# Kernel tuning notes

Hardware: AMD Instinct MI355X
Metric: run time of the kernel (lower is better)

Reference implementation:

```python
import jax, jax.numpy as jnp
import numpy as np

B, S, E, L = 4, 4096, 64, 3
INIT_SCALE = 0.03


def setup_inputs() -> dict:
    key = jax.random.key(0)
    ks = jax.random.split(key, 7)
    return {
        "x": jax.random.normal(ks[0], (B, S, S + 1), dtype=jnp.float32),
        "q_ws": jax.random.normal(ks[1], (L, E, E), dtype=jnp.float32) * INIT_SCALE,
        "k_ws": jax.random.normal(ks[2], (L, E, E), dtype=jnp.float32) * INIT_SCALE,
        "v_ws": jax.random.normal(ks[3], (L, E, E), dtype=jnp.float32) * INIT_SCALE,
        "random_matrix": jax.random.normal(ks[4], (S, E - 1), dtype=jnp.float32) * INIT_SCALE,
        "coeffs_attended": jax.random.normal(ks[5], (S, E), dtype=jnp.float32) * INIT_SCALE,
        "offset": jax.random.normal(ks[6], (1,), dtype=jnp.float32),
    }


def reference(x, q_ws, k_ws, v_ws, random_matrix, coeffs_attended, offset):
    seq_length = random_matrix.shape[0]
    # project first seq_length feature columns, keep the last column raw -> [B, S, E]
    av = jnp.concatenate(
        [jnp.einsum('bsf,fe->bse', x[:, :, :seq_length], random_matrix), x[:, :, -1:]],
        axis=2,
    )

    def layer(av, ws):
        qw, kw, vw = ws
        q = jnp.einsum('bse,ed->bsd', av, qw)   # [B, S, E]
        k = jnp.einsum('bse,ed->bsd', av, kw)
        v = jnp.einsum('bse,ed->bsd', av, vw)
        scores = jax.nn.softmax(jnp.einsum('bqd,bkd->bqk', q, k), axis=-1)  # [B, S, S]
        out = jnp.einsum('bqk,bkd->bqd', scores, v)
        # skip_connections=False: output replaces attended values
        return out, None

    av, _ = jax.lax.scan(layer, av, (q_ws, k_ws, v_ws))
    final = jnp.einsum('bij,ij->b', av, coeffs_attended)  # [B]
    return final + offset[0]
```

## Files before the change

### kernel.cpp

```cpp
#include <hip/hip_runtime.h>

#define SEQ  4096
#define EMB  64
#define NB   4
#define XROW 4097

#define SW(r, c) ((r) * 64 + (((c) ^ ((r) & 7)) << 3))

typedef unsigned short ushort_t;
typedef __attribute__((ext_vector_type(8))) short short8;
typedef __attribute__((ext_vector_type(4))) float floatx4;

union U8 { uint4 u; short8 s8; };

__device__ __forceinline__ ushort_t f2bf(float f) {
    union { float f; unsigned int u; } v; v.f = f;
    unsigned int r = v.u + 0x7FFFu + ((v.u >> 16) & 1u);
    return (ushort_t)(r >> 16);
}
__device__ __forceinline__ uint2 pack4bf(float a, float b, float c, float d) {
    uint2 p;
    p.x = (unsigned)f2bf(a) | ((unsigned)f2bf(b) << 16);
    p.y = (unsigned)f2bf(c) | ((unsigned)f2bf(d) << 16);
    return p;
}

__global__ __launch_bounds__(256) void prep_rmt(const float* __restrict__ rm,
                                                ushort_t* __restrict__ rmT,
                                                float* __restrict__ out,
                                                const float* __restrict__ offset) {
    if (blockIdx.x == 0 && threadIdx.x < NB) out[threadIdx.x] = offset[0];
    int o = (blockIdx.x * 256 + threadIdx.x) * 4;
    int e = o >> 12;
    int f = o & 4095;
    alignas(8) ushort_t t[4];
    t[0] = f2bf((e < 63) ? rm[(size_t)(f + 0) * 63 + e] : 0.f);
    t[1] = f2bf((e < 63) ? rm[(size_t)(f + 1) * 63 + e] : 0.f);
    t[2] = f2bf((e < 63) ? rm[(size_t)(f + 2) * 63 + e] : 0.f);
    t[3] = f2bf((e < 63) ? rm[(size_t)(f + 3) * 63 + e] : 0.f);
    *(uint2*)&rmT[o] = *(uint2*)t;
}

__global__ __launch_bounds__(512) void proj_mfma(const float* __restrict__ x,
        const ushort_t* __restrict__ rmT, float* __restrict__ av) {
    __shared__ ushort_t xs[2][64 * 64];
    __shared__ ushort_t rs[2][64 * 64];
    const int tid = threadIdx.x;
    const int row0 = blockIdx.x * 64;
    const int w = tid >> 6, l = tid & 63;
    const int wg = w >> 2;
    const int wq = w & 3;
    const int t4 = tid & 255;
    const int srow = t4 >> 2, sc = (t4 & 3) * 16;
    const int c0 = (t4 & 3) * 2;
    const int kbase = wg * 2048;
    const int quad = l >> 4, q16 = l & 15;

    floatx4 acc[4];
    #pragma unroll
    for (int i = 0; i < 4; ++i) acc[i] = (floatx4){0.f, 0.f, 0.f, 0.f};

    float px[16];
    short8 pr0, pr1;
    {
        const float* xp = x + (size_t)(row0 + srow) * XROW + kbase + sc;
        #pragma unroll
        for (int i = 0; i < 16; ++i) px[i] = xp[i];
        const ushort_t* rp = rmT + (size_t)srow * SEQ + kbase + sc;
        pr0 = *(const short8*)&rp[0];
        pr1 = *(const short8*)&rp[8];
    }

    for (int k0 = 0; k0 < 2048; k0 += 64) {
        __syncthreads();
        {
            alignas(16) ushort_t tmp[16];
            #pragma unroll
            for (int i = 0; i < 16; ++i) tmp[i] = f2bf(px[i]);
            *(short8*)&xs[wg][SW(srow, c0)]     = *(short8*)&tmp[0];
            *(short8*)&xs[wg][SW(srow, c0 + 1)] = *(short8*)&tmp[8];
            *(short8*)&rs[wg][SW(srow, c0)]     = pr0;
            *(short8*)&rs[wg][SW(srow, c0 + 1)] = pr1;
        }
        __syncthreads();
        if (k0 + 64 < 2048) {
            const float* xp = x + (size_t)(row0 + srow) * XROW + kbase + k0 + 64 + sc;
            #pragma unroll
            for (int i = 0; i < 16; ++i) px[i] = xp[i];
            const ushort_t* rp = rmT + (size_t)srow * SEQ + kbase + k0 + 64 + sc;
            pr0 = *(const short8*)&rp[0];
            pr1 = *(const short8*)&rp[8];
        }
        #pragma unroll
        for (int ksp = 0; ksp < 2; ++ksp) {
            short8 a = *(short8*)&xs[wg][SW(wq * 16 + q16, ksp * 4 + quad)];
            #pragma unroll
            for (int nt = 0; nt < 4; ++nt) {
                short8 bf = *(short8*)&rs[wg][SW(nt * 16 + q16, ksp * 4 + quad)];
                acc[nt] = __builtin_amdgcn_mfma_f32_16x16x32_bf16(a, bf, acc[nt], 0, 0, 0);
            }
        }
    }

    __syncthreads();
    float* poc = (float*)xs;
    if (wg == 1) {
        #pragma unroll
        for (int nt = 0; nt < 4; ++nt)
            #pragma unroll
            for (int r = 0; r < 4; ++r)
                poc[(wq * 16 + quad * 4 + r) * 64 + nt * 16 + q16] = acc[nt][r];
    }
    __syncthreads();
    if (wg == 0) {
        #pragma unroll
        for (int nt = 0; nt < 4; ++nt)
            #pragma unroll
            for (int r = 0; r < 4; ++r) {
                int row = row0 + wq * 16 + quad * 4 + r;
                int col = nt * 16 + q16;
                float v = acc[nt][r] + poc[(wq * 16 + quad * 4 + r) * 64 + col];
                if (col == 63) v = x[(size_t)row * XROW + SEQ];
                av[(size_t)row * EMB + col] = v;
            }
    }
}

__global__ __launch_bounds__(256) void qkv_mfma(const float* __restrict__ av,
        const float* __restrict__ qw, const float* __restrict__ kw,
        const float* __restrict__ vw, ushort_t* __restrict__ Qb,
        ushort_t* __restrict__ Kb, ushort_t* __restrict__ Vt) {
    __shared__ ushort_t avs[64 * 64];
    __shared__ ushort_t wqs[64 * 64], wks[64 * 64], wvs[64 * 64];
    const int tid = threadIdx.x;
    const int row0 = blockIdx.x * 64;
    const int w = tid >> 6, l = tid & 63;
    const int srow = tid >> 2, sc = (tid & 3) * 16;
    const int c0 = (tid & 3) * 2;

    {
        const float* ap = av + (size_t)(row0 + srow) * EMB + sc;
        alignas(16) ushort_t tmp[16];
        #pragma unroll
        for (int i = 0; i < 16; ++i) tmp[i] = f2bf(ap[i]);
        *(short8*)&avs[SW(srow, c0)]     = *(short8*)&tmp[0];
        *(short8*)&avs[SW(srow, c0 + 1)] = *(short8*)&tmp[8];
    }
    {
        alignas(16) ushort_t tq[16], tk[16], tv[16];
        #pragma unroll
        for (int i = 0; i < 16; ++i) {
            int kk = sc + i;
            tq[i] = f2bf(qw[kk * 64 + srow]);
            tk[i] = f2bf(kw[kk * 64 + srow]);
            tv[i] = f2bf(vw[kk * 64 + srow]);
        }
        *(short8*)&wqs[SW(srow, c0)]     = *(short8*)&tq[0];
        *(short8*)&wqs[SW(srow, c0 + 1)] = *(short8*)&tq[8];
        *(short8*)&wks[SW(srow, c0)]     = *(short8*)&tk[0];
        *(short8*)&wks[SW(srow, c0 + 1)] = *(short8*)&tk[8];
        *(short8*)&wvs[SW(srow, c0)]     = *(short8*)&tv[0];
        *(short8*)&wvs[SW(srow, c0 + 1)] = *(short8*)&tv[8];
    }
    __syncthreads();

    floatx4 aq[4], ak[4], avv[4];
    #pragma unroll
    for (int i = 0; i < 4; ++i) {
        aq[i] = (floatx4){0.f, 0.f, 0.f, 0.f};
        ak[i] = aq[i]; avv[i] = aq[i];
    }
    #pragma unroll
    for (int ksp = 0; ksp < 2; ++ksp) {
        short8 a = *(short8*)&avs[SW(w * 16 + (l & 15), ksp * 4 + (l >> 4))];
        #pragma unroll
        for (int nt = 0; nt < 4; ++nt) {
            int bo = SW(nt * 16 + (l & 15), ksp * 4 + (l >> 4));
            aq[nt]  = __builtin_amdgcn_mfma_f32_16x16x32_bf16(a, *(short8*)&wqs[bo], aq[nt], 0, 0, 0);
            ak[nt]  = __builtin_amdgcn_mfma_f32_16x16x32_bf16(a, *(short8*)&wks[bo], ak[nt], 0, 0, 0);
            avv[nt] = __builtin_amdgcn_mfma_f32_16x16x32_bf16(a, *(short8*)&wvs[bo], avv[nt], 0, 0, 0);
        }
    }

    const int b = row0 >> 12;
    #pragma unroll
    for (int nt = 0; nt < 4; ++nt)
        #pragma unroll
        for (int r = 0; r < 4; ++r) {
            int row = row0 + w * 16 + (l >> 4) * 4 + r;
            int col = nt * 16 + (l & 15);
            size_t o = (size_t)row * EMB + col;
            Qb[o] = f2bf(aq[nt][r]);
            Kb[o] = f2bf(ak[nt][r]);
            Vt[((size_t)b * EMB + col) * SEQ + (row & 4095)] = f2bf(avv[nt][r]);
        }
}

__global__ __launch_bounds__(512) void flash_mfma(const ushort_t* __restrict__ Qb,
        const ushort_t* __restrict__ Kb, const ushort_t* __restrict__ Vt,
        float* __restrict__ out) {
    __shared__ ushort_t ks[4][64 * 64];
    __shared__ ushort_t vt[4][64 * 64];
    __shared__ ushort_t psbuf[8 * 2048];
    __shared__ float comb[3][64 * 64];
    __shared__ float lrow[4][64];
    const int tid = threadIdx.x;
    const int w = tid >> 6, l = tid & 63;
    const int wg = w >> 1;
    const int wq = w & 1;
    const int quad = l >> 4, q16 = l & 15;
    const int flat = blockIdx.y * 64 + blockIdx.x;
    const int xcd = flat & 7, slot = flat >> 3;
    const int b = xcd >> 1;
    const int q0 = ((xcd & 1) * 32 + slot) * 64;
    const size_t base  = (size_t)b * SEQ * EMB;
    const size_t vbase = (size_t)b * EMB * SEQ;
    const int qtr  = tid >> 7;
    const int t7   = tid & 127;
    const int srow = t7 >> 1;
    const int hc   = (t7 & 1) * 4;
    ushort_t* ps = &psbuf[w * 2048];

    short8 qf[2][2];
    #pragma unroll
    for (int qh = 0; qh < 2; ++qh)
        #pragma unroll
        for (int ksp = 0; ksp < 2; ++ksp)
            qf[qh][ksp] = *(const short8*)&Qb[base
                + (size_t)(q0 + wq * 32 + qh * 16 + q16) * EMB + ksp * 32 + quad * 8];

    short8 pk[4], pv[4];
    {
        const ushort_t* kp = Kb + base + (size_t)(qtr * 1024 + srow) * EMB + hc * 8;
        const ushort_t* vp = Vt + vbase + (size_t)srow * SEQ + qtr * 1024 + hc * 8;
        #pragma unroll
        for (int j = 0; j < 4; ++j) {
            pk[j] = *(const short8*)(kp + j * 8);
            pv[j] = *(const short8*)(vp + j * 8);
        }
    }

    floatx4 o_acc[2][4];
    #pragma unroll
    for (int qh = 0; qh < 2; ++qh)
        #pragma unroll
        for (int i = 0; i < 4; ++i) o_acc[qh][i] = (floatx4){0.f, 0.f, 0.f, 0.f};
    float lp0 = 0.f, lp1 = 0.f;

    for (int kt0 = 0; kt0 < 1024; kt0 += 64) {
        __syncthreads();
        #pragma unroll
        for (int j = 0; j < 4; ++j) {
            *(short8*)&ks[qtr][SW(srow, hc + j)] = pk[j];
            *(short8*)&vt[qtr][SW(srow, hc + j)] = pv[j];
        }
        __syncthreads();
        if (kt0 + 64 < 1024) {
            const ushort_t* kp = Kb + base + (size_t)(qtr * 1024 + kt0 + 64 + srow) * EMB + hc * 8;
            const ushort_t* vp = Vt + vbase + (size_t)srow * SEQ + qtr * 1024 + kt0 + 64 + hc * 8;
            #pragma unroll
            for (int j = 0; j < 4; ++j) {
                pk[j] = *(const short8*)(kp + j * 8);
                pv[j] = *(const short8*)(vp + j * 8);
            }
        }

        floatx4 s[2][4];
        #pragma unroll
        for (int qh = 0; qh < 2; ++qh)
            #pragma unroll
            for (int nt = 0; nt < 4; ++nt) s[qh][nt] = (floatx4){0.f, 0.f, 0.f, 0.f};
        __builtin_amdgcn_s_setprio(1);
        #pragma unroll
        for (int ksp = 0; ksp < 2; ++ksp) {
            #pragma unroll
            for (int nt = 0; nt < 4; ++nt) {
                short8 a = *(short8*)&ks[wg][SW(nt * 16 + q16, ksp * 4 + quad)];
                s[0][nt] = __builtin_amdgcn_mfma_f32_16x16x32_bf16(a, qf[0][ksp], s[0][nt], 0, 0, 0);
                s[1][nt] = __builtin_amdgcn_mfma_f32_16x16x32_bf16(a, qf[1][ksp], s[1][nt], 0, 0, 0);
            }
        }
        __builtin_amdgcn_s_setprio(0);

        short8 bv[2][4];
        #pragma unroll
        for (int ksp = 0; ksp < 2; ++ksp)
            #pragma unroll
            for (int nt = 0; nt < 4; ++nt)
                bv[ksp][nt] = *(short8*)&vt[wg][SW(nt * 16 + q16, ksp * 4 + quad)];

        #pragma unroll
        for (int nt = 0; nt < 4; ++nt) {
            float p0 = __expf(s[0][nt][0]);
            float p1 = __expf(s[0][nt][1]);
            float p2 = __expf(s[0][nt][2]);
            float p3 = __expf(s[0][nt][3]);
            lp0 += (p0 + p1) + (p2 + p3);
            int g = nt * 4 + quad;
            *(uint2*)&ps[q16 * 64 + ((g ^ q16) & 15) * 4] = pack4bf(p0, p1, p2, p3);
        }
        #pragma unroll
        for (int nt = 0; nt < 4; ++nt) {
            float p0 = __expf(s[1][nt][0]);
            float p1 = __expf(s[1][nt][1]);
            float p2 = __expf(s[1][nt][2]);
            float p3 = __expf(s[1][nt][3]);
            lp1 += (p0 + p1) + (p2 + p3);
            int g = nt * 4 + quad;
            *(uint2*)&ps[1024 + q16 * 64 + ((g ^ q16) & 15) * 4] = pack4bf(p0, p1, p2, p3);
        }
        asm volatile("s_waitcnt lgkmcnt(0)" ::: "memory");

        __builtin_amdgcn_s_setprio(1);
        #pragma unroll
        for (int ksp = 0; ksp < 2; ++ksp) {
            #pragma unroll
            for (int qh = 0; qh < 2; ++qh) {
                int g0 = ksp * 8 + quad * 2;
                uint2 a0 = *(uint2*)&ps[qh * 1024 + q16 * 64 + ((g0 ^ q16) & 15) * 4];
                uint2 a1 = *(uint2*)&ps[qh * 1024 + q16 * 64 + (((g0 + 1) ^ q16) & 15) * 4];
                U8 af;
                af.u.x = a0.x; af.u.y = a0.y; af.u.z = a1.x; af.u.w = a1.y;
                #pragma unroll
                for (int nt = 0; nt < 4; ++nt)
                    o_acc[qh][nt] = __builtin_amdgcn_mfma_f32_16x16x32_bf16(af.s8, bv[ksp][nt], o_acc[qh][nt], 0, 0, 0);
            }
        }
        __builtin_amdgcn_s_setprio(0);
    }

    lp0 += __shfl_xor(lp0, 16);
    lp0 += __shfl_xor(lp0, 32);
    lp1 += __shfl_xor(lp1, 16);
    lp1 += __shfl_xor(lp1, 32);
    if (quad == 0) {
        lrow[wg][wq * 32 + q16]      = lp0;
        lrow[wg][wq * 32 + 16 + q16] = lp1;
    }
    if (wg > 0) {
        #pragma unroll
        for (int qh = 0; qh < 2; ++qh)
            #pragma unroll
            for (int nt = 0; nt < 4; ++nt)
                #pragma unroll
                for (int r = 0; r < 4; ++r)
                    comb[wg - 1][(wq * 32 + qh * 16 + quad * 4 + r) * 64 + nt * 16 + q16]
                        = o_acc[qh][nt][r];
    }
    __syncthreads();
    if (wg == 0) {
        #pragma unroll
        for (int qh = 0; qh < 2; ++qh) {
            float linv[4];
            #pragma unroll
            for (int r = 0; r < 4; ++r) {
                int ql = wq * 32 + qh * 16 + quad * 4 + r;
                linv[r] = 1.f / (lrow[0][ql] + lrow[1][ql] + lrow[2][ql] + lrow[3][ql]);
            }
            #pragma unroll
            for (int nt = 0; nt < 4; ++nt)
                #pragma unroll
                for (int r = 0; r < 4; ++r) {
                    int ql = wq * 32 + qh * 16 + quad * 4 + r;
                    int col = nt * 16 + q16;
                    float v = (o_acc[qh][nt][r] + comb[0][ql * 64 + col]
                               + comb[1][ql * 64 + col] + comb[2][ql * 64 + col]) * linv[r];
                    out[base + (size_t)(q0 + ql) * EMB + col] = v;
                }
        }
    }
}

__global__ __launch_bounds__(256) void reduce_kernel(const float* __restrict__ av,
        const float* __restrict__ coeffs, float* __restrict__ out) {
    const int b = blockIdx.y;
    const size_t base = (size_t)b * SEQ * EMB;
    const int local0 = blockIdx.x * 4096;
    const int tid = threadIdx.x;
    float ssum = 0.f;
    #pragma unroll
    for (int i = 0; i < 4; ++i) {
        int idx = local0 + (tid + i * 256) * 4;
        float4 a = *(const float4*)&av[base + idx];
        float4 c = *(const float4*)&coeffs[idx];
        ssum += a.x * c.x + a.y * c.y + a.z * c.z + a.w * c.w;
    }
    #pragma unroll
    for (int off = 1; off < 64; off <<= 1) ssum += __shfl_xor(ssum, off);
    __shared__ float wsum[4];
    if ((tid & 63) == 0) wsum[tid >> 6] = ssum;
    __syncthreads();
    if (tid == 0)
        atomicAdd(&out[b], wsum[0] + wsum[1] + wsum[2] + wsum[3]);
}

extern "C" void kernel_launch(void* const* d_in, const int* in_sizes, int n_in,
                              void* d_out, int out_size, void* d_ws, size_t ws_size,
                              hipStream_t stream) {
    const float* x      = (const float*)d_in[0];
    const float* q_ws   = (const float*)d_in[1];
    const float* k_ws   = (const float*)d_in[2];
    const float* v_ws   = (const float*)d_in[3];
    const float* rm     = (const float*)d_in[4];
    const float* coeffs = (const float*)d_in[5];
    const float* offset = (const float*)d_in[6];
    float* out = (float*)d_out;
    char* ws = (char*)d_ws;

    float*    AV  = (float*)ws;
    ushort_t* Qb  = (ushort_t*)(ws + 4 * 1024 * 1024);
    ushort_t* Kb  = (ushort_t*)(ws + 6 * 1024 * 1024);
    ushort_t* Vt  = (ushort_t*)(ws + 8 * 1024 * 1024);
    ushort_t* rmT = (ushort_t*)(ws + 10 * 1024 * 1024);

    prep_rmt<<<256, 256, 0, stream>>>(rm, rmT, out, offset);
    proj_mfma<<<256, 512, 0, stream>>>(x, rmT, AV);
    for (int layer = 0; layer < 3; ++layer) {
        qkv_mfma<<<256, 256, 0, stream>>>(AV, q_ws + layer * 4096,
                                          k_ws + layer * 4096, v_ws + layer * 4096,
                                          Qb, Kb, Vt);
        flash_mfma<<<dim3(64, NB), 512, 0, stream>>>(Qb, Kb, Vt, AV);
    }
    reduce_kernel<<<dim3(64, NB), 256, 0, stream>>>(AV, coeffs, out);
}
```

Measured before the change: 524.1 us.

## Fuse QKV projection into projection and flash epilogues, fold final reduction

Removes the standalone qkv kernels and the reduce kernel. The input projection and each attention layer's epilogue now compute the next layer's Q, K and V directly from the bf16 output tile held in shared memory, writing to ping-pong buffers. The last attention layer takes the dot product with the coefficients and atomically adds it to the output. This cuts kernel launches and the fp32 activation round trip through global memory. The cost is extra shared-memory work and syncs in the epilogue, plus reuse of psbuf after an added barrier.

Result: no change. 517.9 us (-1.2%).

```diff
diff --git a/kernel.cpp b/kernel.cpp
--- a/kernel.cpp
+++ b/kernel.cpp
@@ -5,7 +5,8 @@
 #define NB   4
 #define XROW 4097
 
-#define SW(r, c) ((r) * 64 + (((c) ^ ((r) & 7)) << 3))
+#define SW(r, c)    ((r) * 64 + (((c) ^ ((r) & 7)) << 3))
+#define SWE(r, col) ((r) * 64 + (((((col) >> 3)) ^ ((r) & 7)) << 3) + ((col) & 7))
 
 typedef unsigned short ushort_t;
 typedef __attribute__((ext_vector_type(8))) short short8;
@@ -41,10 +42,15 @@
     *(uint2*)&rmT[o] = *(uint2*)t;
 }
 
-__global__ __launch_bounds__(512) void proj_mfma(const float* __restrict__ x,
-        const ushort_t* __restrict__ rmT, float* __restrict__ av) {
+__global__ __launch_bounds__(512) void proj_qkv(const float* __restrict__ x,
+        const ushort_t* __restrict__ rmT,
+        const float* __restrict__ qw, const float* __restrict__ kw,
+        const float* __restrict__ vw,
+        ushort_t* __restrict__ Qo, ushort_t* __restrict__ Ko,
+        ushort_t* __restrict__ Vo) {
     __shared__ ushort_t xs[2][64 * 64];
     __shared__ ushort_t rs[2][64 * 64];
+    __shared__ ushort_t ep[2][64 * 64];
     const int tid = threadIdx.x;
     const int row0 = blockIdx.x * 64;
     const int w = tid >> 6, l = tid & 63;
@@ -111,94 +117,79 @@
             for (int r = 0; r < 4; ++r)
                 poc[(wq * 16 + quad * 4 + r) * 64 + nt * 16 + q16] = acc[nt][r];
     }
+    {
+        const int wrow = tid >> 3, wch = tid & 7;
+        alignas(16) ushort_t tw[8];
+        ushort_t* wdst[3] = { rs[0], rs[1], ep[0] };
+        const float* wsrc[3] = { qw, kw, vw };
+        #pragma unroll
+        for (int m = 0; m < 3; ++m) {
+            #pragma unroll
+            for (int i = 0; i < 8; ++i)
+                tw[i] = f2bf(wsrc[m][(wch * 8 + i) * 64 + wrow]);
+            *(short8*)&wdst[m][SW(wrow, wch)] = *(short8*)tw;
+        }
+    }
     __syncthreads();
+    ushort_t* ot = ep[1];
     if (wg == 0) {
         #pragma unroll
         for (int nt = 0; nt < 4; ++nt)
             #pragma unroll
             for (int r = 0; r < 4; ++r) {
-                int row = row0 + wq * 16 + quad * 4 + r;
+                int ql = wq * 16 + quad * 4 + r;
                 int col = nt * 16 + q16;
-                float v = acc[nt][r] + poc[(wq * 16 + quad * 4 + r) * 64 + col];
-                if (col == 63) v = x[(size_t)row * XROW + SEQ];
-                av[(size_t)row * EMB + col] = v;
-            }
-    }
-}
-
-__global__ __launch_bounds__(256) void qkv_mfma(const float* __restrict__ av,
+                float v = acc[nt][r] + poc[ql * 64 + col];
+                if (col == 63) v = x[(size_t)(row0 + ql) * XROW + SEQ];
+                ot[SWE(ql, col)] = f2bf(v);
+            }
+    }
+    __syncthreads();
+    {
+        const int erow = (w & 3) * 16;
+        floatx4 ra[4], rb[4];
+        #pragma unroll
+        for (int i = 0; i < 4; ++i) {
+            ra[i] = (floatx4){0.f, 0.f, 0.f, 0.f};
+            rb[i] = ra[i];
+        }
+        const ushort_t* wb0 = (w < 4) ? rs[0] : ep[0];
+        #pragma unroll
+        for (int ksp = 0; ksp < 2; ++ksp) {
+            short8 a = *(short8*)&ot[SW(erow + q16, ksp * 4 + quad)];
+            #pragma unroll
+            for (int nt = 0; nt < 4; ++nt) {
+                int bo = SW(nt * 16 + q16, ksp * 4 + quad);
+                ra[nt] = __builtin_amdgcn_mfma_f32_16x16x32_bf16(a, *(short8*)&wb0[bo], ra[nt], 0, 0, 0);
+                if (w < 4)
+                    rb[nt] = __builtin_amdgcn_mfma_f32_16x16x32_bf16(a, *(short8*)&rs[1][bo], rb[nt], 0, 0, 0);
+            }
+        }
+        const int b = row0 >> 12;
+        #pragma unroll
+        for (int nt = 0; nt < 4; ++nt)
+            #pragma unroll
+            for (int r = 0; r < 4; ++r) {
+                int row = row0 + erow + quad * 4 + r;
+                int col = nt * 16 + q16;
+                if (w < 4) {
+                    Qo[(size_t)row * EMB + col] = f2bf(ra[nt][r]);
+                    Ko[(size_t)row * EMB + col] = f2bf(rb[nt][r]);
+                } else {
+                    Vo[((size_t)b * EMB + col) * SEQ + (row & 4095)] = f2bf(ra[nt][r]);
+                }
+            }
+    }
+}
+
+template<int MODE>
+__global__ __launch_bounds__(512) void flash_fused(const ushort_t* __restrict__ Qb,
+        const ushort_t* __restrict__ Kb, const ushort_t* __restrict__ Vt,
         const float* __restrict__ qw, const float* __restrict__ kw,
-        const float* __restrict__ vw, ushort_t* __restrict__ Qb,
-        ushort_t* __restrict__ Kb, ushort_t* __restrict__ Vt) {
-    __shared__ ushort_t avs[64 * 64];
-    __shared__ ushort_t wqs[64 * 64], wks[64 * 64], wvs[64 * 64];
-    const int tid = threadIdx.x;
-    const int row0 = blockIdx.x * 64;
-    const int w = tid >> 6, l = tid & 63;
-    const int srow = tid >> 2, sc = (tid & 3) * 16;
-    const int c0 = (tid & 3) * 2;
-
-    {
-        const float* ap = av + (size_t)(row0 + srow) * EMB + sc;
-        alignas(16) ushort_t tmp[16];
-        #pragma unroll
-        for (int i = 0; i < 16; ++i) tmp[i] = f2bf(ap[i]);
-        *(short8*)&avs[SW(srow, c0)]     = *(short8*)&tmp[0];
-        *(short8*)&avs[SW(srow, c0 + 1)] = *(short8*)&tmp[8];
-    }
-    {
-        alignas(16) ushort_t tq[16], tk[16], tv[16];
-        #pragma unroll
-        for (int i = 0; i < 16; ++i) {
-            int kk = sc + i;
-            tq[i] = f2bf(qw[kk * 64 + srow]);
-            tk[i] = f2bf(kw[kk * 64 + srow]);
-            tv[i] = f2bf(vw[kk * 64 + srow]);
-        }
-        *(short8*)&wqs[SW(srow, c0)]     = *(short8*)&tq[0];
-        *(short8*)&wqs[SW(srow, c0 + 1)] = *(short8*)&tq[8];
-        *(short8*)&wks[SW(srow, c0)]     = *(short8*)&tk[0];
-        *(short8*)&wks[SW(srow, c0 + 1)] = *(short8*)&tk[8];
-        *(short8*)&wvs[SW(srow, c0)]     = *(short8*)&tv[0];
-        *(short8*)&wvs[SW(srow, c0 + 1)] = *(short8*)&tv[8];
-    }
-    __syncthreads();
-
-    floatx4 aq[4], ak[4], avv[4];
-    #pragma unroll
-    for (int i = 0; i < 4; ++i) {
-        aq[i] = (floatx4){0.f, 0.f, 0.f, 0.f};
-        ak[i] = aq[i]; avv[i] = aq[i];
-    }
-    #pragma unroll
-    for (int ksp = 0; ksp < 2; ++ksp) {
-        short8 a = *(short8*)&avs[SW(w * 16 + (l & 15), ksp * 4 + (l >> 4))];
-        #pragma unroll
-        for (int nt = 0; nt < 4; ++nt) {
-            int bo = SW(nt * 16 + (l & 15), ksp * 4 + (l >> 4));
-            aq[nt]  = __builtin_amdgcn_mfma_f32_16x16x32_bf16(a, *(short8*)&wqs[bo], aq[nt], 0, 0, 0);
-            ak[nt]  = __builtin_amdgcn_mfma_f32_16x16x32_bf16(a, *(short8*)&wks[bo], ak[nt], 0, 0, 0);
-            avv[nt] = __builtin_amdgcn_mfma_f32_16x16x32_bf16(a, *(short8*)&wvs[bo], avv[nt], 0, 0, 0);
-        }
-    }
-
-    const int b = row0 >> 12;
-    #pragma unroll
-    for (int nt = 0; nt < 4; ++nt)
-        #pragma unroll
-        for (int r = 0; r < 4; ++r) {
-            int row = row0 + w * 16 + (l >> 4) * 4 + r;
-            int col = nt * 16 + (l & 15);
-            size_t o = (size_t)row * EMB + col;
-            Qb[o] = f2bf(aq[nt][r]);
-            Kb[o] = f2bf(ak[nt][r]);
-            Vt[((size_t)b * EMB + col) * SEQ + (row & 4095)] = f2bf(avv[nt][r]);
-        }
-}
-
-__global__ __launch_bounds__(512) void flash_mfma(const ushort_t* __restrict__ Qb,
-        const ushort_t* __restrict__ Kb, const ushort_t* __restrict__ Vt,
-        float* __restrict__ out) {
+        const float* __restrict__ vw,
+        ushort_t* __restrict__ Qo, ushort_t* __restrict__ Ko,
+        ushort_t* __restrict__ Vo,
+        const float* __restrict__ coeffs, float* __restrict__ out) {
     __shared__ ushort_t ks[4][64 * 64];
     __shared__ ushort_t vt[4][64 * 64];
     __shared__ ushort_t psbuf[8 * 2048];
@@ -333,6 +324,7 @@
     lp0 += __shfl_xor(lp0, 32);
     lp1 += __shfl_xor(lp1, 16);
     lp1 += __shfl_xor(lp1, 32);
+    __syncthreads();
     if (quad == 0) {
         lrow[wg][wq * 32 + q16]      = lp0;
         lrow[wg][wq * 32 + 16 + q16] = lp1;
@@ -347,7 +339,21 @@
                     comb[wg - 1][(wq * 32 + qh * 16 + quad * 4 + r) * 64 + nt * 16 + q16]
                         = o_acc[qh][nt][r];
     }
+    if constexpr (MODE == 0) {
+        const int wrow = tid >> 3, wch = tid & 7;
+        alignas(16) ushort_t tw[8];
+        const float* wsrc[3] = { qw, kw, vw };
+        #pragma unroll
+        for (int m = 0; m < 3; ++m) {
+            #pragma unroll
+            for (int i = 0; i < 8; ++i)
+                tw[i] = f2bf(wsrc[m][(wch * 8 + i) * 64 + wrow]);
+            *(short8*)&psbuf[m * 4096 + SW(wrow, wch)] = *(short8*)tw;
+        }
+    }
     __syncthreads();
+    ushort_t* ot = &psbuf[3 * 4096];
+    float pdot = 0.f;
     if (wg == 0) {
         #pragma unroll
         for (int qh = 0; qh < 2; ++qh) {
@@ -365,33 +371,55 @@
                     int col = nt * 16 + q16;
                     float v = (o_acc[qh][nt][r] + comb[0][ql * 64 + col]
                                + comb[1][ql * 64 + col] + comb[2][ql * 64 + col]) * linv[r];
-                    out[base + (size_t)(q0 + ql) * EMB + col] = v;
+                    if constexpr (MODE == 1)
+                        pdot += v * coeffs[(size_t)(q0 + ql) * EMB + col];
+                    else
+                        ot[SWE(ql, col)] = f2bf(v);
                 }
         }
     }
-}
-
-__global__ __launch_bounds__(256) void reduce_kernel(const float* __restrict__ av,
-        const float* __restrict__ coeffs, float* __restrict__ out) {
-    const int b = blockIdx.y;
-    const size_t base = (size_t)b * SEQ * EMB;
-    const int local0 = blockIdx.x * 4096;
-    const int tid = threadIdx.x;
-    float ssum = 0.f;
-    #pragma unroll
-    for (int i = 0; i < 4; ++i) {
-        int idx = local0 + (tid + i * 256) * 4;
-        float4 a = *(const float4*)&av[base + idx];
-        float4 c = *(const float4*)&coeffs[idx];
-        ssum += a.x * c.x + a.y * c.y + a.z * c.z + a.w * c.w;
-    }
-    #pragma unroll
-    for (int off = 1; off < 64; off <<= 1) ssum += __shfl_xor(ssum, off);
-    __shared__ float wsum[4];
-    if ((tid & 63) == 0) wsum[tid >> 6] = ssum;
-    __syncthreads();
-    if (tid == 0)
-        atomicAdd(&out[b], wsum[0] + wsum[1] + wsum[2] + wsum[3]);
+    if constexpr (MODE == 1) {
+        if (wg == 0) {
+            #pragma unroll
+            for (int off = 1; off < 64; off <<= 1) pdot += __shfl_xor(pdot, off);
+            if (l == 0) atomicAdd(&out[b], pdot);
+        }
+        return;
+    } else {
+        __syncthreads();
+        const int erow = (w & 3) * 16;
+        floatx4 ra[4], rb[4];
+        #pragma unroll
+        for (int i = 0; i < 4; ++i) {
+            ra[i] = (floatx4){0.f, 0.f, 0.f, 0.f};
+            rb[i] = ra[i];
+        }
+        const ushort_t* wb0 = (w < 4) ? &psbuf[0] : &psbuf[2 * 4096];
+        #pragma unroll
+        for (int ksp = 0; ksp < 2; ++ksp) {
+            short8 a = *(short8*)&ot[SW(erow + q16, ksp * 4 + quad)];
+            #pragma unroll
+            for (int nt = 0; nt < 4; ++nt) {
+                int bo = SW(nt * 16 + q16, ksp * 4 + quad);
+                ra[nt] = __builtin_amdgcn_mfma_f32_16x16x32_bf16(a, *(short8*)&wb0[bo], ra[nt], 0, 0, 0);
+                if (w < 4)
+                    rb[nt] = __builtin_amdgcn_mfma_f32_16x16x32_bf16(a, *(short8*)&psbuf[4096 + bo], rb[nt], 0, 0, 0);
+            }
+        }
+        #pragma unroll
+        for (int nt = 0; nt < 4; ++nt)
+            #pragma unroll
+            for (int r = 0; r < 4; ++r) {
+                int row = q0 + erow + quad * 4 + r;
+                int col = nt * 16 + q16;
+                if (w < 4) {
+                    Qo[base + (size_t)row * EMB + col] = f2bf(ra[nt][r]);
+                    Ko[base + (size_t)row * EMB + col] = f2bf(rb[nt][r]);
+                } else {
+                    Vo[vbase + (size_t)col * SEQ + row] = f2bf(ra[nt][r]);
+                }
+            }
+    }
 }
 
 extern "C" void kernel_launch(void* const* d_in, const int* in_sizes, int n_in,
@@ -407,19 +435,21 @@
     float* out = (float*)d_out;
     char* ws = (char*)d_ws;
 
-    float*    AV  = (float*)ws;
-    ushort_t* Qb  = (ushort_t*)(ws + 4 * 1024 * 1024);
-    ushort_t* Kb  = (ushort_t*)(ws + 6 * 1024 * 1024);
-    ushort_t* Vt  = (ushort_t*)(ws + 8 * 1024 * 1024);
-    ushort_t* rmT = (ushort_t*)(ws + 10 * 1024 * 1024);
+    const size_t MB = 1024 * 1024;
+    ushort_t* QbA = (ushort_t*)(ws + 0 * MB);
+    ushort_t* KbA = (ushort_t*)(ws + 2 * MB);
+    ushort_t* VtA = (ushort_t*)(ws + 4 * MB);
+    ushort_t* QbB = (ushort_t*)(ws + 6 * MB);
+    ushort_t* KbB = (ushort_t*)(ws + 8 * MB);
+    ushort_t* VtB = (ushort_t*)(ws + 10 * MB);
+    ushort_t* rmT = (ushort_t*)(ws + 12 * MB);
 
     prep_rmt<<<256, 256, 0, stream>>>(rm, rmT, out, offset);
-    proj_mfma<<<256, 512, 0, stream>>>(x, rmT, AV);
-    for (int layer = 0; layer < 3; ++layer) {
-        qkv_mfma<<<256, 256, 0, stream>>>(AV, q_ws + layer * 4096,
-                                          k_ws + layer * 4096, v_ws + layer * 4096,
-                                          Qb, Kb, Vt);
-        flash_mfma<<<dim3(64, NB), 512, 0, stream>>>(Qb, Kb, Vt, AV);
-    }
-    reduce_kernel<<<dim3(64, NB), 256, 0, stream>>>(AV, coeffs, out);
-}
+    proj_qkv<<<256, 512, 0, stream>>>(x, rmT, q_ws, k_ws, v_ws, QbA, KbA, VtA);
+    flash_fused<0><<<dim3(64, NB), 512, 0, stream>>>(QbA, KbA, VtA,
+        q_ws + 4096, k_ws + 4096, v_ws + 4096, QbB, KbB, VtB, nullptr, nullptr);
+    flash_fused<0><<<dim3(64, NB), 512, 0, stream>>>(QbB, KbB, VtB,
+        q_ws + 8192, k_ws + 8192, v_ws + 8192, QbA, KbA, VtA, nullptr, nullptr);
+    flash_fused<1><<<dim3(64, NB), 512, 0, stream>>>(QbA, KbA, VtA,
+        nullptr, nullptr, nullptr, nullptr, nullptr, nullptr, coeffs, out);
+}
```
